# Performance work log

Hardware: AMD Instinct MI355X
Metric: run time of the kernel (lower is better)

Reference implementation:

```python
import jax, jax.numpy as jnp
from jax import lax
import numpy as np

B, T, C = 2048, 512, 32  # batch, max_seq_len, num_tags


def setup_inputs() -> dict:
    key = jax.random.key(0)
    k1, k2, k3, k4 = jax.random.split(key, 4)
    logits = jax.random.normal(k1, (B, T, C), dtype=jnp.float32)
    sequence_length = jax.random.randint(k2, (B,), 1, T + 1, dtype=jnp.int32)
    labels = jax.random.randint(k3, (B, T), 0, C, dtype=jnp.int32)
    # learned CRF transition matrix (orthogonal init approximated by normal)
    transitions = jax.random.normal(k4, (C, C), dtype=jnp.float32)
    return dict(logits=logits, sequence_length=sequence_length,
                labels=labels, transitions=transitions)


def _viterbi_decode(logits, transitions, seq_len):
    """tfa_text.crf_decode: returns highest-scoring tag sequence [B, T] int32."""
    Bn, Tn, Cn = logits.shape
    identity_bp = jnp.arange(Cn, dtype=jnp.int32)[None, :]  # carries tag through padding

    def fwd(state, xs):  # state: [B, C] viterbi scores
        logit_t, t = xs
        scores = state[:, :, None] + transitions[None]       # [B, C_prev, C_cur]
        cand = logit_t + jnp.max(scores, axis=1)             # [B, C]
        bp = jnp.argmax(scores, axis=1).astype(jnp.int32)    # [B, C] best prev tag
        active = (t < seq_len)[:, None]
        return (jnp.where(active, cand, state),
                jnp.where(active, bp, identity_bp))

    xs = (jnp.swapaxes(logits[:, 1:], 0, 1), jnp.arange(1, Tn))
    final_state, bps = lax.scan(fwd, logits[:, 0], xs)       # bps: [T-1, B, C]
    last_tag = jnp.argmax(final_state, axis=-1).astype(jnp.int32)  # [B]

    def back(tag, bp):  # tag at t+1 -> tag at t
        prev = jnp.take_along_axis(bp, tag[:, None], axis=1)[:, 0]
        return prev, tag

    first_tag, later_tags = lax.scan(back, last_tag, bps, reverse=True)
    tags = jnp.concatenate([first_tag[None], later_tags], axis=0).T  # [B, T]
    valid = jnp.arange(Tn)[None, :] < seq_len[:, None]
    return jnp.where(valid, tags, 0)


def _crf_log_likelihood(logits, labels, transitions, seq_len):
    """tfa_text.crf_log_likelihood: per-example log-likelihood [B]."""
    Bn, Tn, Cn = logits.shape

    # --- log partition via forward algorithm ---
    def fwd(alpha, xs):
        logit_t, t = xs
        new = jax.nn.logsumexp(alpha[:, :, None] + transitions[None], axis=1) + logit_t
        active = (t < seq_len)[:, None]
        return jnp.where(active, new, alpha), None

    xs = (jnp.swapaxes(logits[:, 1:], 0, 1), jnp.arange(1, Tn))
    alpha, _ = lax.scan(fwd, logits[:, 0], xs)
    log_norm = jax.nn.logsumexp(alpha, axis=-1)  # [B]

    # --- score of gold label sequence ---
    pos = jnp.arange(Tn)
    mask = (pos[None, :] < seq_len[:, None]).astype(logits.dtype)          # [B, T]
    unary = jnp.sum(
        jnp.take_along_axis(logits, labels[..., None], axis=2)[..., 0] * mask,
        axis=1)
    pair_mask = (pos[None, :-1] < (seq_len - 1)[:, None]).astype(logits.dtype)
    binary = jnp.sum(transitions[labels[:, :-1], labels[:, 1:]] * pair_mask, axis=1)

    return unary + binary - log_norm


def reference(logits, sequence_length, labels, transitions):
    # training=True path: labels clamped to >= 0 (already non-negative here)
    labels = jnp.maximum(labels, 0)
    decode_tags = _viterbi_decode(logits, transitions, sequence_length)
    log_likelihood = _crf_log_likelihood(logits, labels, transitions, sequence_length)
    loss = jnp.mean(-log_likelihood)  # recorded via add_loss in the original
    return decode_tags, loss
```

## Files before the change

### kernel.cpp

```cpp
#include <hip/hip_runtime.h>
#include <math.h>

#define BB 2048
#define TT 512
#define CC 32

#if __has_builtin(__builtin_amdgcn_exp2f)
#define EXP2F __builtin_amdgcn_exp2f
#else
#define EXP2F exp2f
#endif
#if __has_builtin(__builtin_amdgcn_logf)
#define LOG2F __builtin_amdgcn_logf
#else
#define LOG2F log2f
#endif

#define LOG2E 1.4426950408889634f
#define LN2   0.6931471805599453f

__global__ void zero_loss_kernel(float* __restrict__ out) {
  if (threadIdx.x == 0) out[(size_t)BB * TT] = 0.0f;
}

__global__ void schedule_kernel(const int* __restrict__ seqlen,
                                int* __restrict__ perm,
                                float* __restrict__ out) {
  __shared__ int s[TT];
  __shared__ int off[TT];
  const int tid = threadIdx.x;
  if (tid == 0) out[(size_t)BB * TT] = 0.0f;
  s[tid] = 0;
  __syncthreads();
  for (int b = tid; b < BB; b += TT) atomicAdd(&s[seqlen[b] - 1], 1);
  __syncthreads();
  for (int d = 1; d < TT; d <<= 1) {
    int v = s[tid] + ((tid + d < TT) ? s[tid + d] : 0);
    __syncthreads();
    s[tid] = v;
    __syncthreads();
  }
  off[tid] = (tid + 1 < TT) ? s[tid + 1] : 0;
  __syncthreads();
  for (int b = tid; b < BB; b += TT) {
    int pos = atomicAdd(&off[seqlen[b] - 1], 1);
    perm[pos] = b;
  }
}

#define ROR(dst, src, K)                                                     \
  dst = __int_as_float(__builtin_amdgcn_update_dpp(                          \
      0, __float_as_int(src), 0x120 | (K), 0xF, 0xF, false));

__device__ __forceinline__ float xor16f(float x, int lane) {
#if __has_builtin(__builtin_amdgcn_permlane16_swap)
  auto r = __builtin_amdgcn_permlane16_swap(__float_as_uint(x),
                                            __float_as_uint(x), false, false);
  return __uint_as_float((lane & 16) ? r[0] : r[1]);
#else
  return __int_as_float(
      __builtin_amdgcn_ds_swizzle(__float_as_int(x), 0x401F));
#endif
}
__device__ __forceinline__ float xor32f(float x, int lane) {
#if __has_builtin(__builtin_amdgcn_permlane32_swap)
  auto r = __builtin_amdgcn_permlane32_swap(__float_as_uint(x),
                                            __float_as_uint(x), false, false);
  return __uint_as_float((lane & 32) ? r[0] : r[1]);
#else
  return __shfl_xor(x, 32);
#endif
}
__device__ __forceinline__ int xor32i(int x, int lane) {
#if __has_builtin(__builtin_amdgcn_permlane32_swap)
  auto r = __builtin_amdgcn_permlane32_swap((unsigned)x, (unsigned)x,
                                            false, false);
  return (int)((lane & 32) ? r[0] : r[1]);
#else
  return __shfl_xor(x, 32);
#endif
}

__global__ __launch_bounds__(128, 4) void crf_kernel(
    const float* __restrict__ logits,
    const int*   __restrict__ seqlen,
    const int*   __restrict__ labels,
    const float* __restrict__ trans,
    float*       __restrict__ out,
    const int*   __restrict__ perm)
{
  __shared__ __align__(16) unsigned char bp_s[(TT - 1) * CC];
  __shared__ unsigned char tag_s[TT];

  const int lane = threadIdx.x & 63;
  const int wv   = threadIdx.x >> 6;
  const int k    = blockIdx.x;

  const int bs0 = perm ? perm[k] : k;
  const int bs1 = perm ? perm[BB - 1 - k] : -1;

  const int i  = lane & 15;
  const int c  = lane & 31;
  const int r  = (lane >> 4) & 1;
  const int pr = (lane < 32) ? r : 1 - r;

  if (wv == 0) {
    float tr2[16];
    int   pidx[16];
#pragma unroll
    for (int kk = 0; kk < 16; ++kk) {
      int p = pr * 16 + ((i - kk) & 15);
      pidx[kk] = p;
      tr2[kk] = trans[p * CC + c];
    }

    for (int sq = 0; sq < 2; ++sq) {
      const int b = sq ? bs1 : bs0;
      if (b < 0) break;
      const int len = seqlen[b];
      const float* lg = logits + (size_t)b * TT * CC;
      const size_t bT = (size_t)b * TT;
      const float* lgc = lg + c;

      float av = lg[c];

      auto vstep = [&](int t, float logit_c) {
        float base = (lane < 32) ? av : xor16f(av, lane);
        float S[16];
        float x;
        S[0] = base + tr2[0];
        ROR(x, base, 1);  S[1]  = x + tr2[1];
        ROR(x, base, 2);  S[2]  = x + tr2[2];
        ROR(x, base, 3);  S[3]  = x + tr2[3];
        ROR(x, base, 4);  S[4]  = x + tr2[4];
        ROR(x, base, 5);  S[5]  = x + tr2[5];
        ROR(x, base, 6);  S[6]  = x + tr2[6];
        ROR(x, base, 7);  S[7]  = x + tr2[7];
        ROR(x, base, 8);  S[8]  = x + tr2[8];
        ROR(x, base, 9);  S[9]  = x + tr2[9];
        ROR(x, base, 10); S[10] = x + tr2[10];
        ROR(x, base, 11); S[11] = x + tr2[11];
        ROR(x, base, 12); S[12] = x + tr2[12];
        ROR(x, base, 13); S[13] = x + tr2[13];
        ROR(x, base, 14); S[14] = x + tr2[14];
        ROR(x, base, 15); S[15] = x + tr2[15];

        float m8[8];
#pragma unroll
        for (int kk = 0; kk < 8; ++kk) m8[kk] = fmaxf(S[kk], S[kk + 8]);
#pragma unroll
        for (int kk = 0; kk < 4; ++kk) m8[kk] = fmaxf(m8[kk], m8[kk + 4]);
        float best = fmaxf(fmaxf(m8[0], m8[2]), fmaxf(m8[1], m8[3]));

        int t8[16];
#pragma unroll
        for (int kk = 0; kk < 16; ++kk)
          t8[kk] = (S[kk] == best) ? pidx[kk] : 63;
#pragma unroll
        for (int kk = 0; kk < 8; ++kk) t8[kk] = min(t8[kk], t8[kk + 8]);
#pragma unroll
        for (int kk = 0; kk < 4; ++kk) t8[kk] = min(t8[kk], t8[kk + 4]);
        int bi = min(min(t8[0], t8[2]), min(t8[1], t8[3]));

        float ov = xor32f(best, lane);
        int   oi = xor32i(bi, lane);
        bool take = (ov > best) || (ov == best && oi < bi);
        best = take ? ov : best;
        int bpi = take ? oi : bi;
        av = logit_c + best;

        if (lane < 32) bp_s[(t - 1) * CC + c] = (unsigned char)bpi;
      };

      float Abk[8], Bbk[8];
      auto loadB = [&](float (&bk)[8], int t0) {
#pragma unroll
        for (int s = 0; s < 8; ++s) {
          int tt = t0 + s; tt = tt < len ? tt : len - 1;
          bk[s] = lgc[tt * CC];
        }
      };
      auto runB = [&](float (&bk)[8], int t0) {
#pragma unroll
        for (int s = 0; s < 8; ++s) {
          int tt = t0 + s;
          if (tt < len) vstep(tt, bk[s]);
        }
      };
      loadB(Abk, 1);
      for (int t0 = 1; t0 < len; t0 += 16) {
        loadB(Bbk, t0 + 8);
        runB(Abk, t0);
        if (t0 + 8 < len) {
          loadB(Abk, t0 + 16);
          runB(Bbk, t0 + 8);
        }
      }

      float v = av; int idx = c;
#pragma unroll
      for (int d = 1; d < 32; d <<= 1) {
        float v2 = __shfl_xor(v, d, 32);
        int   i2 = __shfl_xor(idx, d, 32);
        if (v2 > v || (v2 == v && i2 < idx)) { v = v2; idx = i2; }
      }

      if (lane == 0) {
        int tag = idx;
        tag_s[len - 1] = (unsigned char)tag;
        const uint4* bp4 = (const uint4*)bp_s;
        uint4 Ra[3], Rb[3];
#pragma unroll
        for (int kk = 0; kk < 3; ++kk) {
          int rr = len - 2 - kk;
          if (rr >= 0) { Ra[kk] = bp4[2 * rr]; Rb[kk] = bp4[2 * rr + 1]; }
        }
#pragma unroll 4
        for (int tt = len - 1; tt > 0; --tt) {
          uint4 ua = Ra[0], ub = Rb[0];
          Ra[0] = Ra[1]; Rb[0] = Rb[1];
          Ra[1] = Ra[2]; Rb[1] = Rb[2];
          int rr = tt - 4;
          if (rr >= 0) { Ra[2] = bp4[2 * rr]; Rb[2] = bp4[2 * rr + 1]; }
          uint4 u4;
          u4.x = (tag & 16) ? ub.x : ua.x;
          u4.y = (tag & 16) ? ub.y : ua.y;
          u4.z = (tag & 16) ? ub.z : ua.z;
          u4.w = (tag & 16) ? ub.w : ua.w;
          unsigned lo = (tag & 8) ? u4.z : u4.x;
          unsigned hi = (tag & 8) ? u4.w : u4.y;
          unsigned u1 = (tag & 4) ? hi : lo;
          tag = (int)((u1 >> ((tag & 3) * 8)) & 0xffu);
          tag_s[tt - 1] = (unsigned char)tag;
        }
      }

#pragma unroll
      for (int j = 0; j < 8; ++j) {
        int tt = lane + 64 * j;
        float val = (tt < len) ? (float)tag_s[tt] : 0.0f;
        out[bT + tt] = val;
      }
    }

  } else {
    float E[16];
#pragma unroll
    for (int kk = 0; kk < 16; ++kk) {
      int p = pr * 16 + ((i - kk) & 15);
      E[kk] = EXP2F(trans[p * CC + c] * LOG2E);
    }

    float loss_acc = 0.0f;

    for (int sq = 0; sq < 2; ++sq) {
      const int b = sq ? bs1 : bs0;
      if (b < 0) break;
      const int len = seqlen[b];
      const float* lg = logits + (size_t)b * TT * CC;
      const int* lab = labels + (size_t)b * TT;
      const float* lgc = lg + c;

      float P   = EXP2F(lg[c] * LOG2E);
      float Acc = 0.0f;

      auto fstep = [&](float raw_logit) {
        float el = EXP2F(raw_logit * LOG2E);
        float base = (lane < 32) ? P : xor16f(P, lane);
        float x;
        float a0 = base * E[0];
        ROR(x, base, 1);  float a1 = x * E[1];
        ROR(x, base, 2);  float a2 = x * E[2];
        ROR(x, base, 3);  float a3 = x * E[3];
        ROR(x, base, 4);  a0 = fmaf(x, E[4],  a0);
        ROR(x, base, 5);  a1 = fmaf(x, E[5],  a1);
        ROR(x, base, 6);  a2 = fmaf(x, E[6],  a2);
        ROR(x, base, 7);  a3 = fmaf(x, E[7],  a3);
        ROR(x, base, 8);  a0 = fmaf(x, E[8],  a0);
        ROR(x, base, 9);  a1 = fmaf(x, E[9],  a1);
        ROR(x, base, 10); a2 = fmaf(x, E[10], a2);
        ROR(x, base, 11); a3 = fmaf(x, E[11], a3);
        ROR(x, base, 12); a0 = fmaf(x, E[12], a0);
        ROR(x, base, 13); a1 = fmaf(x, E[13], a1);
        ROR(x, base, 14); a2 = fmaf(x, E[14], a2);
        ROR(x, base, 15); a3 = fmaf(x, E[15], a3);
        float part = (a0 + a1) + (a2 + a3);
        float oth  = xor32f(part, lane);
        P = el * (part + oth);
      };

      auto renorm = [&]() {
        float m = P, y;
        ROR(y, m, 8); m = fmaxf(m, y);
        ROR(y, m, 4); m = fmaxf(m, y);
        ROR(y, m, 2); m = fmaxf(m, y);
        ROR(y, m, 1); m = fmaxf(m, y);
        m = fmaxf(m, xor16f(m, lane));
        int e = (int)(__float_as_uint(m) >> 23) - 127;
        P = ldexpf(P, -e);
        Acc += (float)e;
      };

      float Abk[8], Bbk[8];
      auto loadB = [&](float (&bk)[8], int t0) {
#pragma unroll
        for (int s = 0; s < 8; ++s) {
          int tt = t0 + s; tt = tt < len ? tt : len - 1;
          bk[s] = lgc[tt * CC];
        }
      };
      auto runB = [&](float (&bk)[8], int t0) {
#pragma unroll
        for (int s = 0; s < 8; ++s) {
          int tt = t0 + s;
          if (tt < len) {
            fstep(bk[s]);
            if ((tt & 3) == 0) renorm();
          }
        }
      };
      loadB(Abk, 1);
      for (int t0 = 1; t0 < len; t0 += 16) {
        loadB(Bbk, t0 + 8);
        runB(Abk, t0);
        if (t0 + 8 < len) {
          loadB(Abk, t0 + 16);
          runB(Bbk, t0 + 8);
        }
      }

      float uacc = 0.0f, bacc = 0.0f;
#pragma unroll
      for (int j = 0; j < 8; ++j) {
        int tt = lane + 64 * j;
        if (tt < len) {
          int lt = lab[tt];
          uacc += lg[tt * CC + lt];
          if (tt + 1 < len) {
            int ln = lab[tt + 1];
            bacc += trans[lt * CC + ln];
          }
        }
      }
#pragma unroll
      for (int d = 32; d >= 1; d >>= 1) {
        uacc += __shfl_xor(uacc, d);
        bacc += __shfl_xor(bacc, d);
      }

      float ss = P, y2;
      ROR(y2, ss, 8); ss += y2;
      ROR(y2, ss, 4); ss += y2;
      ROR(y2, ss, 2); ss += y2;
      ROR(y2, ss, 1); ss += y2;
      ss += xor16f(ss, lane);
      float log_norm = LN2 * (Acc + LOG2F(ss));

      loss_acc += (uacc + bacc - log_norm);
    }

    if (lane == 0) {
      atomicAdd(out + (size_t)BB * TT, loss_acc * (-1.0f / BB));
    }
  }
}

extern "C" void kernel_launch(void* const* d_in, const int* in_sizes, int n_in,
                              void* d_out, int out_size, void* d_ws, size_t ws_size,
                              hipStream_t stream) {
  const float* logits = (const float*)d_in[0];
  const int*   seqlen = (const int*)d_in[1];
  const int*   labels = (const int*)d_in[2];
  const float* trans  = (const float*)d_in[3];
  float* out = (float*)d_out;

  if (d_ws != nullptr && ws_size >= BB * sizeof(int)) {
    int* perm = (int*)d_ws;
    schedule_kernel<<<1, TT, 0, stream>>>(seqlen, perm, out);
    crf_kernel<<<dim3(BB / 2), dim3(128), 0, stream>>>(
        logits, seqlen, labels, trans, out, perm);
  } else {
    zero_loss_kernel<<<1, 64, 0, stream>>>(out);
    crf_kernel<<<dim3(BB), dim3(128), 0, stream>>>(
        logits, seqlen, labels, trans, out, nullptr);
  }
}
```

Before: 409.7 us.

## Compose backpointers four steps ahead during Viterbi forward to shorten backtrace chain

During the forward Viterbi pass, every fourth step each tag composes the previous three backpointer steps with ds_bpermute and stores a packed 4-step jump table in shared memory. The serial single-lane backtrace can then follow one dependent load per four timesteps instead of one per step, cutting the latency-bound chain. The max/argmin trees are also rebalanced into 3-way groups, and launch bounds drop to 2 waves per EU. In exchange the forward pass gains extra permutes and LDS traffic on its critical path, plus 16KB more shared memory, which may lower occupancy.

```diff
diff --git a/kernel.cpp b/kernel.cpp
--- a/kernel.cpp
+++ b/kernel.cpp
@@ -81,7 +81,7 @@
 #endif
 }
 
-__global__ __launch_bounds__(128, 4) void crf_kernel(
+__global__ __launch_bounds__(128, 2) void crf_kernel(
     const float* __restrict__ logits,
     const int*   __restrict__ seqlen,
     const int*   __restrict__ labels,
@@ -90,6 +90,7 @@
     const int*   __restrict__ perm)
 {
   __shared__ __align__(16) unsigned char bp_s[(TT - 1) * CC];
+  __shared__ __align__(16) unsigned gp_s[(TT / 4) * CC];
   __shared__ unsigned char tag_s[TT];
 
   const int lane = threadIdx.x & 63;
@@ -124,7 +125,7 @@
 
       float av = lg[c];
 
-      auto vstep = [&](int t, float logit_c) {
+      auto vstep = [&](int t, float logit_c) -> int {
         float base = (lane < 32) ? av : xor16f(av, lane);
         float S[16];
         float x;
@@ -145,22 +146,24 @@
         ROR(x, base, 14); S[14] = x + tr2[14];
         ROR(x, base, 15); S[15] = x + tr2[15];
 
-        float m8[8];
-#pragma unroll
-        for (int kk = 0; kk < 8; ++kk) m8[kk] = fmaxf(S[kk], S[kk + 8]);
-#pragma unroll
-        for (int kk = 0; kk < 4; ++kk) m8[kk] = fmaxf(m8[kk], m8[kk + 4]);
-        float best = fmaxf(fmaxf(m8[0], m8[2]), fmaxf(m8[1], m8[3]));
+        float a = fmaxf(fmaxf(S[0], S[1]), S[2]);
+        float bq = fmaxf(fmaxf(S[3], S[4]), S[5]);
+        float cq = fmaxf(fmaxf(S[6], S[7]), S[8]);
+        float dq = fmaxf(fmaxf(S[9], S[10]), S[11]);
+        float eq = fmaxf(fmaxf(S[12], S[13]), S[14]);
+        float best = fmaxf(fmaxf(fmaxf(a, bq), fmaxf(cq, dq)),
+                           fmaxf(eq, S[15]));
 
         int t8[16];
 #pragma unroll
         for (int kk = 0; kk < 16; ++kk)
           t8[kk] = (S[kk] == best) ? pidx[kk] : 63;
-#pragma unroll
-        for (int kk = 0; kk < 8; ++kk) t8[kk] = min(t8[kk], t8[kk + 8]);
-#pragma unroll
-        for (int kk = 0; kk < 4; ++kk) t8[kk] = min(t8[kk], t8[kk + 4]);
-        int bi = min(min(t8[0], t8[2]), min(t8[1], t8[3]));
+        int ma = min(min(t8[0], t8[1]), t8[2]);
+        int mb = min(min(t8[3], t8[4]), t8[5]);
+        int mc = min(min(t8[6], t8[7]), t8[8]);
+        int md = min(min(t8[9], t8[10]), t8[11]);
+        int me = min(min(t8[12], t8[13]), t8[14]);
+        int bi = min(min(min(ma, mb), min(mc, md)), min(me, t8[15]));
 
         float ov = xor32f(best, lane);
         int   oi = xor32i(bi, lane);
@@ -170,6 +173,7 @@
         av = logit_c + best;
 
         if (lane < 32) bp_s[(t - 1) * CC + c] = (unsigned char)bpi;
+        return bpi;
       };
 
       float Abk[8], Bbk[8];
@@ -181,10 +185,22 @@
         }
       };
       auto runB = [&](float (&bk)[8], int t0) {
+        int h1 = 0, h2 = 0, h3 = 0;
 #pragma unroll
         for (int s = 0; s < 8; ++s) {
           int tt = t0 + s;
-          if (tt < len) vstep(tt, bk[s]);
+          if (tt < len) {
+            int bpi = vstep(tt, bk[s]);
+            if ((tt & 3) == 0) {
+              int m2 = __builtin_amdgcn_ds_bpermute(bpi << 2, h1);
+              int m3 = __builtin_amdgcn_ds_bpermute(m2 << 2, h2);
+              int m4 = __builtin_amdgcn_ds_bpermute(m3 << 2, h3);
+              unsigned packed = (unsigned)bpi | ((unsigned)m2 << 8) |
+                                ((unsigned)m3 << 16) | ((unsigned)m4 << 24);
+              if (lane < 32) gp_s[((tt >> 2) - 1) * CC + c] = packed;
+            }
+            h3 = h2; h2 = h1; h1 = bpi;
+          }
         }
       };
       loadB(Abk, 1);
@@ -207,31 +223,21 @@
 
       if (lane == 0) {
         int tag = idx;
-        tag_s[len - 1] = (unsigned char)tag;
-        const uint4* bp4 = (const uint4*)bp_s;
-        uint4 Ra[3], Rb[3];
-#pragma unroll
-        for (int kk = 0; kk < 3; ++kk) {
-          int rr = len - 2 - kk;
-          if (rr >= 0) { Ra[kk] = bp4[2 * rr]; Rb[kk] = bp4[2 * rr + 1]; }
-        }
-#pragma unroll 4
-        for (int tt = len - 1; tt > 0; --tt) {
-          uint4 ua = Ra[0], ub = Rb[0];
-          Ra[0] = Ra[1]; Rb[0] = Rb[1];
-          Ra[1] = Ra[2]; Rb[1] = Rb[2];
-          int rr = tt - 4;
-          if (rr >= 0) { Ra[2] = bp4[2 * rr]; Rb[2] = bp4[2 * rr + 1]; }
-          uint4 u4;
-          u4.x = (tag & 16) ? ub.x : ua.x;
-          u4.y = (tag & 16) ? ub.y : ua.y;
-          u4.z = (tag & 16) ? ub.z : ua.z;
-          u4.w = (tag & 16) ? ub.w : ua.w;
-          unsigned lo = (tag & 8) ? u4.z : u4.x;
-          unsigned hi = (tag & 8) ? u4.w : u4.y;
-          unsigned u1 = (tag & 4) ? hi : lo;
-          tag = (int)((u1 >> ((tag & 3) * 8)) & 0xffu);
-          tag_s[tt - 1] = (unsigned char)tag;
+        int t = len - 1;
+        tag_s[t] = (unsigned char)tag;
+        while (t > 0 && (t & 3) != 0) {
+          tag = bp_s[(t - 1) * CC + tag];
+          --t;
+          tag_s[t] = (unsigned char)tag;
+        }
+        while (t >= 4) {
+          unsigned u = gp_s[((t >> 2) - 1) * CC + tag];
+          tag_s[t - 1] = (unsigned char)(u & 255);
+          tag_s[t - 2] = (unsigned char)((u >> 8) & 255);
+          tag_s[t - 3] = (unsigned char)((u >> 16) & 255);
+          tag = (int)(u >> 24);
+          tag_s[t - 4] = (unsigned char)tag;
+          t -= 4;
         }
       }
 
```

Measured after the change: 377.3 us. 1.09x faster.
